# Kernel optimization log

Hardware: AMD Instinct MI355X
Metric: run time of the kernel (lower is better)

The kernel has to match this reference:

```python
import jax, jax.numpy as jnp
jax.config.update("jax_enable_x64", True)
import numpy as np

B_, H_, W_, O_ = 8, 96, 96, 8
STRIDES = 1


def generate_px_coordinates(shape, coord_K, strides=1):
    # coord_K: [B,2,2]; row 0 = per-axis scale, row 1 = per-axis offset
    H, W = shape
    u = jnp.arange(W, dtype=coord_K.dtype)[None, None, :]
    v = jnp.arange(H, dtype=coord_K.dtype)[None, :, None]
    u = u * strides * coord_K[:, 0, 0][:, None, None] + coord_K[:, 1, 0][:, None, None]
    v = v * strides * coord_K[:, 0, 1][:, None, None] + coord_K[:, 1, 1][:, None, None]
    B = coord_K.shape[0]
    return jnp.broadcast_to(u, (B, H, W)), jnp.broadcast_to(v, (B, H, W))


def matrix_A(obj, TCR):
    # obj: [B,H,W,O,3]; TCR: [B,4,4] -> A: [B,H,W,O,4,13]
    p1 = obj[..., 0:1]
    p2 = obj[..., 1:2]
    p3 = obj[..., 2:3]
    one = jnp.ones_like(p1)
    T1 = TCR[:, None, None, None, :, 0]
    T2 = TCR[:, None, None, None, :, 1]
    T3 = TCR[:, None, None, None, :, 2]
    T4 = TCR[:, None, None, None, :, 3]
    return jnp.stack((p1 * T1, p2 * T1, p3 * T1,
                      p1 * T2, p2 * T2, p3 * T2,
                      p1 * T3, p2 * T3, p3 * T3,
                      one * T4, one * T1, one * T2, one * T3), axis=-1)


def matrix_B(shape, camera_matrix, coord_K, strides=1):
    # -> [B,H,W,2,4]
    u, v = generate_px_coordinates(shape, coord_K, strides)
    coords = jnp.stack([u, v], axis=-1)[..., None]  # [B,H,W,2,1]
    left4 = -jnp.eye(2, dtype=camera_matrix.dtype)[None, None, None] \
            * camera_matrix[:, None, None, :2, :2]  # [B,H,W,2,2]
    Bn, H, W = u.shape
    left4 = jnp.broadcast_to(left4, (Bn, H, W, 2, 2))
    d1_2 = coords - camera_matrix[:, None, None, :2, 2:3]  # [B,H,W,2,1]
    return jnp.concatenate([left4, d1_2, jnp.zeros_like(d1_2)], axis=-1)


def setup_inputs() -> dict:
    key = jax.random.key(0)
    k1, k2, k3, k4 = jax.random.split(key, 4)
    obj = jax.random.normal(k1, (B_, H_, W_, O_, 3), dtype=jnp.float32)
    w_pixel = jax.random.normal(k2, (B_, H_, W_, O_, 4), dtype=jnp.float32)
    camera_matrix = jax.random.normal(k3, (B_, 3, 3), dtype=jnp.float32)
    coord_K = jax.random.uniform(k4, (B_, 2, 2), dtype=jnp.float32)
    return {"obj": obj, "w_pixel": w_pixel,
            "camera_matrix": camera_matrix, "coord_K": coord_K}


def reference(obj, w_pixel, camera_matrix, coord_K):
    B, H, W, O = obj.shape[:4]
    Wp = w_pixel.reshape(B, H, W, O, 2, 2)
    TCR = jnp.broadcast_to(jnp.eye(4, dtype=obj.dtype), (B, 4, 4))
    A = matrix_A(obj, TCR)                                  # [B,H,W,O,4,13]
    Bm = matrix_B((H, W), camera_matrix, coord_K, STRIDES)  # [B,H,W,2,4]
    BA = jnp.einsum('bxyij,bxyojk->bxyoik', Bm, A)          # [B,H,W,O,2,13]
    MRow = jnp.matmul(Wp, BA)                               # [B,H,W,O,2,13]
    num_eq = 2 * H * W
    M = jnp.transpose(MRow, (0, 3, 1, 2, 4, 5)).reshape(B, O, num_eq, 13)
    M = M.astype(jnp.float64)
    return jnp.matmul(jnp.swapaxes(M, -1, -2), M)           # [B,O,13,13]
```

## Files before the change

kernel.cpp:

```cpp
#include <hip/hip_runtime.h>

#define B_ 8
#define H_ 96
#define W_ 96
#define O_ 8
#define HW_ (H_ * W_)
#define NT 576
#define NCH 32
#define PPB (HW_ / NCH)
#define PG (NT / O_)
#define ITERS (PPB / PG)
#define NWAVE (NT / 64)

__global__ __launch_bounds__(NT) void mtm_kernel(
    const float* __restrict__ obj,
    const float* __restrict__ wpx,
    const float* __restrict__ cam,
    const float* __restrict__ ck,
    float* __restrict__ out)
{
    const int chunk = blockIdx.x;
    const int b     = blockIdx.y;

    const float* cm = cam + b * 9;
    const float* k4 = ck  + b * 4;
    const float a   = -cm[0];
    const float c   = -cm[4];
    const float k00 = k4[0];
    const float k01 = k4[1];
    const float Bu  = k4[2] - cm[2];
    const float Bv  = k4[3] - cm[5];

    const int o  = threadIdx.x & 7;
    const int pg = threadIdx.x >> 3;

    float acc[64];
#pragma unroll
    for (int s = 0; s < 64; ++s) acc[s] = 0.f;

#pragma unroll
    for (int it = 0; it < ITERS; ++it) {
        const int p = chunk * PPB + it * PG + pg;
        const int h = p / W_;
        const int w = p - h * W_;
        const int slot = (b * HW_ + p) * O_ + o;

        const float* ob = obj + (size_t)slot * 3;
        const float p1 = ob[0], p2 = ob[1], p3 = ob[2];
        const float4 wp = *(const float4*)(wpx + (size_t)slot * 4);

        const float du = fmaf((float)w, k00, Bu);
        const float dv = fmaf((float)h, k01, Bv);

        const float x00 = wp.x * a;
        const float x01 = wp.y * c;
        const float x02 = fmaf(wp.x, du, wp.y * dv);
        const float x10 = wp.z * a;
        const float x11 = wp.w * c;
        const float x12 = fmaf(wp.z, du, wp.w * dv);

        float Xa[6];
        Xa[0] = fmaf(x00, x00, x10 * x10);
        Xa[1] = fmaf(x00, x01, x10 * x11);
        Xa[2] = fmaf(x00, x02, x10 * x12);
        Xa[3] = fmaf(x01, x01, x11 * x11);
        Xa[4] = fmaf(x01, x02, x11 * x12);
        Xa[5] = fmaf(x02, x02, x12 * x12);

        float Q[10];
        Q[0] = p1 * p1; Q[1] = p1 * p2; Q[2] = p1 * p3; Q[3] = p1;
        Q[4] = p2 * p2; Q[5] = p2 * p3; Q[6] = p2;
        Q[7] = p3 * p3; Q[8] = p3;
        Q[9] = 1.f;

#pragma unroll
        for (int ij = 0; ij < 6; ++ij) {
#pragma unroll
            for (int kl = 0; kl < 10; ++kl)
                acc[ij * 10 + kl] = fmaf(Xa[ij], Q[kl], acc[ij * 10 + kl]);
        }
    }

    const int j  = pg & 7;
    const bool b0 = (j & 1) != 0;
    const bool b1 = (j & 2) != 0;
    const bool b2 = (j & 4) != 0;

    float Br[32];
#pragma unroll
    for (int k = 0; k < 32; ++k) {
        const float keep = b0 ? acc[32 + k] : acc[k];
        const float send = b0 ? acc[k]      : acc[32 + k];
        Br[k] = keep + __shfl_xor(send, 8, 64);
    }
    float Cr[16];
#pragma unroll
    for (int k = 0; k < 16; ++k) {
        const float keep = b1 ? Br[16 + k] : Br[k];
        const float send = b1 ? Br[k]      : Br[16 + k];
        Cr[k] = keep + __shfl_xor(send, 16, 64);
    }
    float Dr[8];
#pragma unroll
    for (int k = 0; k < 8; ++k) {
        const float keep = b2 ? Cr[8 + k] : Cr[k];
        const float send = b2 ? Cr[k]     : Cr[8 + k];
        Dr[k] = keep + __shfl_xor(send, 32, 64);
    }

    __shared__ float lds[NWAVE * 512];
    __shared__ float Sf[512];
    const int wave = threadIdx.x >> 6;
    const int rev  = ((j & 1) << 2) | (j & 2) | ((j >> 2) & 1);
    float* dst = &lds[wave * 512 + o * 64 + rev * 8];
    *(float4*)(dst)     = make_float4(Dr[0], Dr[1], Dr[2], Dr[3]);
    *(float4*)(dst + 4) = make_float4(Dr[4], Dr[5], Dr[6], Dr[7]);
    __syncthreads();

    if (threadIdx.x < 512) {
        float v = 0.f;
#pragma unroll
        for (int w = 0; w < NWAVE; ++w) v += lds[w * 512 + threadIdx.x];
        Sf[threadIdx.x] = v;
    }
    __syncthreads();

    const int offs = (chunk * 191) % 1352;
    for (int n = threadIdx.x; n < 8 * 169; n += NT) {
        int t = n + offs;
        if (t >= 1352) t -= 1352;
        const int oo = t / 169;
        const int e  = t - oo * 169;
        const int r  = e / 13;
        const int cc = e - r * 13;
        float* dp = out + ((size_t)(b * O_ + oo) * 169 + e);
        if (r == 9 || cc == 9) {
            if (chunk == 0) *dp = 0.f;
            continue;
        }
        int i, k, jj_, l;
        if (r < 9)  { i = r / 3;   k = r - i * 3; }   else { i = r - 10;   k = 3; }
        if (cc < 9) { jj_ = cc / 3; l = cc - jj_ * 3; } else { jj_ = cc - 10; l = 3; }
        const int ii = i < jj_ ? i : jj_, jm = i < jj_ ? jj_ : i;
        const int kk = k < l ? k : l,     lm = k < l ? l : k;
        const int ijIdx = ii * (5 - ii) / 2 + jm;
        const int klIdx = kk * (7 - kk) / 2 + lm;
        atomicAdd(dp, Sf[oo * 64 + ijIdx * 10 + klIdx]);
    }
}

extern "C" void kernel_launch(void* const* d_in, const int* in_sizes, int n_in,
                              void* d_out, int out_size, void* d_ws, size_t ws_size,
                              hipStream_t stream) {
    const float* obj = (const float*)d_in[0];
    const float* wpx = (const float*)d_in[1];
    const float* cam = (const float*)d_in[2];
    const float* ck  = (const float*)d_in[3];
    float* out = (float*)d_out;

    mtm_kernel<<<dim3(NCH, B_), dim3(NT), 0, stream>>>(obj, wpx, cam, ck, out);
}
```

Before: 74.19 us.

## Prefetch all per-thread inputs upfront and reduce waves via LDS atomics

All global loads (obj, w_pixel) and pixel-coordinate math for every iteration are issued before the accumulation loop, so memory latency overlaps instead of stalling each iteration. The cross-wave reduction no longer stages per-wave partials in a large LDS buffer followed by a serial sum. Instead each thread atomically adds its 8 partials into a single zero-initialised shared array, with a rotated index order to spread bank conflicts. This raises register pressure from holding ITERS sets of inputs and relies on LDS float atomics, whose summation order is non-deterministic.

```diff
diff --git a/kernel.cpp b/kernel.cpp
--- a/kernel.cpp
+++ b/kernel.cpp
@@ -22,6 +22,9 @@
     const int chunk = blockIdx.x;
     const int b     = blockIdx.y;
 
+    __shared__ float Sf[512];
+    if (threadIdx.x < 512) Sf[threadIdx.x] = 0.f;
+
     const float* cm = cam + b * 9;
     const float* k4 = ck  + b * 4;
     const float a   = -cm[0];
@@ -34,23 +37,33 @@
     const int o  = threadIdx.x & 7;
     const int pg = threadIdx.x >> 3;
 
+    float p1v[ITERS], p2v[ITERS], p3v[ITERS];
+    float4 wpv[ITERS];
+    float duv[ITERS], dvv[ITERS];
+#pragma unroll
+    for (int it = 0; it < ITERS; ++it) {
+        const int p = chunk * PPB + it * PG + pg;
+        const int h = p / W_;
+        const int w = p - h * W_;
+        const int slot = (b * HW_ + p) * O_ + o;
+        const float* ob = obj + (size_t)slot * 3;
+        p1v[it] = ob[0];
+        p2v[it] = ob[1];
+        p3v[it] = ob[2];
+        wpv[it] = *(const float4*)(wpx + (size_t)slot * 4);
+        duv[it] = fmaf((float)w, k00, Bu);
+        dvv[it] = fmaf((float)h, k01, Bv);
+    }
+
     float acc[64];
 #pragma unroll
     for (int s = 0; s < 64; ++s) acc[s] = 0.f;
 
 #pragma unroll
     for (int it = 0; it < ITERS; ++it) {
-        const int p = chunk * PPB + it * PG + pg;
-        const int h = p / W_;
-        const int w = p - h * W_;
-        const int slot = (b * HW_ + p) * O_ + o;
-
-        const float* ob = obj + (size_t)slot * 3;
-        const float p1 = ob[0], p2 = ob[1], p3 = ob[2];
-        const float4 wp = *(const float4*)(wpx + (size_t)slot * 4);
-
-        const float du = fmaf((float)w, k00, Bu);
-        const float dv = fmaf((float)h, k01, Bv);
+        const float p1 = p1v[it], p2 = p2v[it], p3 = p3v[it];
+        const float4 wp = wpv[it];
+        const float du = duv[it], dv = dvv[it];
 
         const float x00 = wp.x * a;
         const float x01 = wp.y * c;
@@ -108,20 +121,12 @@
         Dr[k] = keep + __shfl_xor(send, 32, 64);
     }
 
-    __shared__ float lds[NWAVE * 512];
-    __shared__ float Sf[512];
-    const int wave = threadIdx.x >> 6;
-    const int rev  = ((j & 1) << 2) | (j & 2) | ((j >> 2) & 1);
-    float* dst = &lds[wave * 512 + o * 64 + rev * 8];
-    *(float4*)(dst)     = make_float4(Dr[0], Dr[1], Dr[2], Dr[3]);
-    *(float4*)(dst + 4) = make_float4(Dr[4], Dr[5], Dr[6], Dr[7]);
+    const int rev = ((j & 1) << 2) | (j & 2) | ((j >> 2) & 1);
     __syncthreads();
-
-    if (threadIdx.x < 512) {
-        float v = 0.f;
 #pragma unroll
-        for (int w = 0; w < NWAVE; ++w) v += lds[w * 512 + threadIdx.x];
-        Sf[threadIdx.x] = v;
+    for (int k = 0; k < 8; ++k) {
+        const int kk = (k + o) & 7;
+        atomicAdd(&Sf[o * 64 + rev * 8 + kk], Dr[kk]);
     }
     __syncthreads();
 
```

Measured after the change: 79.54 us. 1.07x slower.
